# Kernel tuning notes

Measured on AMD Instinct MI355X. Metric: run time of the kernel, lower is better.

The kernel has to match this reference:

```python
import jax, jax.numpy as jnp
import numpy as np

NUM_CLUSTERS = 128  # max cluster id per point cloud (segments per cloud)
EPS = 1e-12         # matches torch F.normalize eps


def setup_inputs() -> dict:
    key = jax.random.key(0)
    k1, k2, k3 = jax.random.split(key, 3)
    K, d, N, M = 64, 320, 2048, NUM_CLUSTERS
    feat = jax.random.normal(k1, (K, d, N), dtype=jnp.float32)
    # binary foreground mask per point (float, as in the torch code: label.float())
    label = (jax.random.uniform(k2, (K, N)) < 0.5).astype(jnp.float32)
    cluster_label = jax.random.randint(k3, (K, N), 0, M, dtype=jnp.int32)
    return {"feat": feat, "label": label, "cluster_label": cluster_label}


def reference(feat, label, cluster_label):
    """Fused aggregate_cluster_one_class + detect_clean_cluster_one_class.

    feat:          (K, d, N) per-point features
    label:         (K, N)    binary class mask (float)
    cluster_label: (K, N)    int cluster ids in [0, NUM_CLUSTERS)
    Returns (cluster_means (K*M, d), sim_score (K*M,), clean_mask (K*M,) float).
    Clusters are laid out as fixed K*M segments; non-class / empty clusters are
    masked out (feature & weight = 0), matching the variable-length gathers of
    the original via masking instead of dynamic shapes.
    """
    K, d, N = feat.shape
    M = NUM_CLUSTERS
    S = K * M

    # Offset cluster ids per cloud -> one flat segment reduce (scatter_add/mean)
    seg = (cluster_label.astype(jnp.int32) + jnp.arange(K, dtype=jnp.int32)[:, None] * M).reshape(-1)  # (K*N,)
    fx = feat.transpose(0, 2, 1).reshape(K * N, d)                     # (K*N, d)

    counts = jax.ops.segment_sum(jnp.ones((K * N,), jnp.float32), seg, num_segments=S)  # scatter_add of ones
    feat_sum = jax.ops.segment_sum(fx, seg, num_segments=S)                              # (S, d)
    lbl_sum = jax.ops.segment_sum(label.reshape(-1), seg, num_segments=S)

    denom = jnp.maximum(counts, 1.0)
    cluster_means = feat_sum / denom[:, None]   # scatter_mean(feat)
    lbl_mean = lbl_sum / denom                  # scatter_mean(label)

    # class clusters: mean label > 0.5 (and cluster non-empty)
    cls_mask = (lbl_mean > 0.5) & (counts > 0)  # (S,) bool

    # ---- detect_clean_cluster_one_class ----
    norm = jnp.linalg.norm(cluster_means, axis=1, keepdims=True)       # L2 over feature dim
    fn = cluster_means / jnp.maximum(norm, EPS)
    fn = jnp.where(cls_mask[:, None], fn, 0.0)                         # drop non-class clusters

    sizes = counts * cls_mask.astype(jnp.float32)
    weight = sizes / jnp.maximum(jnp.max(sizes), 1.0)                  # size / size.max()

    sim_mtx = fn @ fn.T                                                # (S, S) cosine similarities
    sim_score = sim_mtx @ weight                                       # weighted row-sum

    n_valid = jnp.maximum(jnp.sum(cls_mask.astype(jnp.float32)), 1.0)
    mean_score = jnp.sum(sim_score * cls_mask) / n_valid
    clean_mask = (sim_score > mean_score) & cls_mask

    return cluster_means, sim_score, clean_mask.astype(jnp.float32)
```

## Files before the change

kernel.cpp:

```cpp
#include <hip/hip_runtime.h>
#include <hip/hip_bf16.h>

#define KC 64
#define DD 320
#define NP 2048
#define MC 128
#define SS (KC * MC)
#define EPSV 1e-12f

#define CHUNKF 20
#define NCHUNKF 16
#define GFEAT 4
#define NGROUP 5
#define TILEW 2176

__global__ __launch_bounds__(256) void sortstats_kernel(
    const float* __restrict__ label,
    const int* __restrict__ clab,
    unsigned short* __restrict__ spos_ws,
    int* __restrict__ starts_ws,
    float* __restrict__ cls_ws,
    float* __restrict__ sizes_ws,
    unsigned* __restrict__ maxbits,
    float* __restrict__ nvalid)
{
    const int k = blockIdx.x;
    const int tid = threadIdx.x;

    __shared__ int   s_cnt[MC];
    __shared__ float s_lbl[MC];
    __shared__ int   s_scan[MC + 1];
    __shared__ float s_red[256];

    if (tid < MC) { s_cnt[tid] = 0; s_lbl[tid] = 0.f; }
    __syncthreads();

    int id[8], rk[8];
#pragma unroll
    for (int i = 0; i < 8; ++i) {
        const int p = i * 256 + tid;
        id[i] = clab[k * NP + p];
        rk[i] = atomicAdd(&s_cnt[id[i]], 1);
        unsafeAtomicAdd(&s_lbl[id[i]], label[k * NP + p]);
    }
    __syncthreads();

    if (tid < MC) s_scan[tid + 1] = s_cnt[tid];
    if (tid == 0) s_scan[0] = 0;
    __syncthreads();
    for (int off = 1; off < MC; off <<= 1) {
        int v = 0;
        if (tid < MC && (tid + 1) > off) v = s_scan[tid + 1 - off];
        __syncthreads();
        if (tid < MC) s_scan[tid + 1] += v;
        __syncthreads();
    }

    float localmax = 0.f, localval = 0.f;
    if (tid < MC) {
        const int c = s_cnt[tid];
        const float lm = s_lbl[tid] / fmaxf((float)c, 1.f);
        const bool is = (lm > 0.5f) && (c > 0);
        const float sz = is ? (float)c : 0.f;
        cls_ws[k * MC + tid] = is ? 1.f : 0.f;
        sizes_ws[k * MC + tid] = sz;
        localmax = sz;
        localval = is ? 1.f : 0.f;
    }
    s_red[tid] = localmax;
    __syncthreads();
    for (int off = 128; off > 0; off >>= 1) {
        if (tid < off) s_red[tid] = fmaxf(s_red[tid], s_red[tid + off]);
        __syncthreads();
    }
    if (tid == 0) atomicMax(maxbits, __float_as_uint(s_red[0]));
    __syncthreads();
    s_red[tid] = localval;
    __syncthreads();
    for (int off = 128; off > 0; off >>= 1) {
        if (tid < off) s_red[tid] += s_red[tid + off];
        __syncthreads();
    }
    if (tid == 0) unsafeAtomicAdd(nvalid, s_red[0]);

    for (int i = tid; i < MC + 1; i += 256) starts_ws[k * (MC + 1) + i] = s_scan[i];
#pragma unroll
    for (int i = 0; i < 8; ++i) {
        const int p = i * 256 + tid;
        const int sp0 = s_scan[id[i]] + rk[i];
        spos_ws[k * NP + p] = (unsigned short)(sp0 + (sp0 >> 4));
    }
}

__global__ __launch_bounds__(512) void means_kernel(
    const float* __restrict__ feat,
    const unsigned short* __restrict__ spos_ws,
    const int* __restrict__ starts_ws,
    float* __restrict__ means_out)
{
    const int k = blockIdx.x;
    const int chunk = blockIdx.y;
    const int tid = threadIdx.x;

    __shared__ float s_tile[2][GFEAT][TILEW];
    __shared__ unsigned short s_sp[NP];
    __shared__ int s_starts[MC + 1];

    {
        const unsigned* spg = (const unsigned*)(spos_ws + (size_t)k * NP);
        for (int i = tid; i < NP / 2; i += 512) ((unsigned*)s_sp)[i] = spg[i];
        if (tid < MC + 1) s_starts[tid] = starts_ws[k * (MC + 1) + tid];
    }
    __syncthreads();

    const int m = tid & 127;
    const int r = tid >> 7;

    unsigned short sp[16];
#pragma unroll
    for (int q = 0; q < 4; ++q) {
        const int p0 = (m + 128 * q) * 4;
#pragma unroll
        for (int e = 0; e < 4; ++e) sp[4 * q + e] = s_sp[p0 + e];
    }

    const int st = s_starts[m];
    const int en = s_starts[m + 1];
    const float invd = 1.0f / fmaxf((float)(en - st), 1.0f);

    const float* fb = feat + (size_t)k * DD * NP + (size_t)chunk * CHUNKF * NP;
    float regsum[NGROUP];
    float4 ld[4];

    {
        const float4* src = (const float4*)(fb + (size_t)r * NP);
#pragma unroll
        for (int q = 0; q < 4; ++q) ld[q] = src[m + 128 * q];
#pragma unroll
        for (int q = 0; q < 4; ++q) {
            s_tile[0][r][sp[4 * q + 0]] = ld[q].x;
            s_tile[0][r][sp[4 * q + 1]] = ld[q].y;
            s_tile[0][r][sp[4 * q + 2]] = ld[q].z;
            s_tile[0][r][sp[4 * q + 3]] = ld[q].w;
        }
    }
    __syncthreads();

#pragma unroll
    for (int g = 0; g < NGROUP; ++g) {
        const int cur = g & 1;
        if (g + 1 < NGROUP) {
            const float4* src = (const float4*)(fb + (size_t)((g + 1) * GFEAT + r) * NP);
#pragma unroll
            for (int q = 0; q < 4; ++q) ld[q] = src[m + 128 * q];
        }
        float acc = 0.f;
        for (int qq = st; qq < en; ++qq) {
            acc += s_tile[cur][r][qq + (qq >> 4)];
        }
        regsum[g] = acc;
        if (g + 1 < NGROUP) {
#pragma unroll
            for (int q = 0; q < 4; ++q) {
                s_tile[cur ^ 1][r][sp[4 * q + 0]] = ld[q].x;
                s_tile[cur ^ 1][r][sp[4 * q + 1]] = ld[q].y;
                s_tile[cur ^ 1][r][sp[4 * q + 2]] = ld[q].z;
                s_tile[cur ^ 1][r][sp[4 * q + 3]] = ld[q].w;
            }
        }
        __syncthreads();
    }

    float* mrow = means_out + (size_t)(k * MC + m) * DD + chunk * CHUNKF;
#pragma unroll
    for (int g = 0; g < NGROUP; ++g) mrow[g * GFEAT + r] = regsum[g] * invd;
}

__global__ __launch_bounds__(256) void norm_v_kernel(
    const float* __restrict__ means,
    const float* __restrict__ cls,
    const float* __restrict__ sizes,
    const unsigned* __restrict__ maxbits,
    float* __restrict__ rw,
    float* __restrict__ v)
{
    const int wid = threadIdx.x >> 6;
    const int lane = threadIdx.x & 63;
    const int seg0 = blockIdx.x * 64 + wid * 16;
    const float rmx = 1.0f / fmaxf(__uint_as_float(*maxbits), 1.0f);

    float vacc[5] = {0, 0, 0, 0, 0};
    for (int i = 0; i < 16; ++i) {
        const int s = seg0 + i;
        const float* row = means + (size_t)s * DD;
        float val[5];
        float ssum = 0.f;
#pragma unroll
        for (int r = 0; r < 5; ++r) {
            val[r] = row[r * 64 + lane];
            ssum = fmaf(val[r], val[r], ssum);
        }
#pragma unroll
        for (int off = 32; off > 0; off >>= 1) ssum += __shfl_xor(ssum, off, 64);
        const float inv = 1.f / fmaxf(sqrtf(ssum), EPSV);
        const float rwv = cls[s] * inv;
        if (lane == 0) rw[s] = rwv;
        const float coef = sizes[s] * rmx * rwv;
#pragma unroll
        for (int r = 0; r < 5; ++r) vacc[r] = fmaf(coef, val[r], vacc[r]);
    }

    __shared__ float vtmp[4][DD];
#pragma unroll
    for (int r = 0; r < 5; ++r) vtmp[wid][r * 64 + lane] = vacc[r];
    __syncthreads();
    for (int j = threadIdx.x; j < DD; j += 256) {
        unsafeAtomicAdd(&v[j], vtmp[0][j] + vtmp[1][j] + vtmp[2][j] + vtmp[3][j]);
    }
}

__global__ __launch_bounds__(256) void sim_kernel(
    const float* __restrict__ means,
    const float* __restrict__ rw,
    const float* __restrict__ v,
    float* __restrict__ sim_out,
    float* __restrict__ simtotal)
{
    const int wid = threadIdx.x >> 6;
    const int lane = threadIdx.x & 63;
    const int seg0 = blockIdx.x * 64 + wid * 16;

    float vreg[5];
#pragma unroll
    for (int r = 0; r < 5; ++r) vreg[r] = v[r * 64 + lane];

    float lsum = 0.f;
    for (int i = 0; i < 16; ++i) {
        const int s = seg0 + i;
        const float* row = means + (size_t)s * DD;
        float dot = 0.f;
#pragma unroll
        for (int r = 0; r < 5; ++r) dot = fmaf(row[r * 64 + lane], vreg[r], dot);
#pragma unroll
        for (int off = 32; off > 0; off >>= 1) dot += __shfl_xor(dot, off, 64);
        const float sim = rw[s] * dot;
        if (lane == 0) {
            sim_out[s] = sim;
            lsum += sim;
        }
    }
    __shared__ float stmp[4];
    if (lane == 0) stmp[wid] = lsum;
    __syncthreads();
    if (threadIdx.x == 0)
        unsafeAtomicAdd(simtotal, stmp[0] + stmp[1] + stmp[2] + stmp[3]);
}

__global__ __launch_bounds__(256) void clean_kernel(
    const float* __restrict__ sim,
    const float* __restrict__ cls,
    const float* __restrict__ simtotal,
    const float* __restrict__ nvalid,
    float* __restrict__ clean_out)
{
    const float mean = simtotal[0] / fmaxf(nvalid[0], 1.f);
    const int tid = threadIdx.x;
    for (int i = tid; i < SS / 4; i += 256) {
        const float4 s4 = ((const float4*)sim)[i];
        const float4 c4 = ((const float4*)cls)[i];
        float4 o;
        o.x = (s4.x > mean && c4.x != 0.f) ? 1.f : 0.f;
        o.y = (s4.y > mean && c4.y != 0.f) ? 1.f : 0.f;
        o.z = (s4.z > mean && c4.z != 0.f) ? 1.f : 0.f;
        o.w = (s4.w > mean && c4.w != 0.f) ? 1.f : 0.f;
        ((float4*)clean_out)[i] = o;
    }
}

extern "C" void kernel_launch(void* const* d_in, const int* in_sizes, int n_in,
                              void* d_out, int out_size, void* d_ws, size_t ws_size,
                              hipStream_t stream) {
    const float* feat  = (const float*)d_in[0];
    const float* label = (const float*)d_in[1];
    const int*   clab  = (const int*)d_in[2];

    float* out       = (float*)d_out;
    float* means_out = out;
    float* sim_out   = out + (size_t)SS * DD;
    float* clean_out = sim_out + SS;

    float* ws = (float*)d_ws;
    unsigned* maxbits = (unsigned*)&ws[0];
    float* nvalid     = &ws[1];
    float* simtotal   = &ws[2];
    float* v          = &ws[4];
    float* cls        = &ws[352];
    float* sizes      = &ws[352 + SS];
    float* rw         = &ws[352 + 2 * SS];
    int*   starts     = (int*)&ws[352 + 3 * SS];
    unsigned short* spos = (unsigned short*)&ws[352 + 3 * SS + KC * (MC + 1)];

    hipMemsetAsync(d_ws, 0, 324 * sizeof(float), stream);

    sortstats_kernel<<<KC, 256, 0, stream>>>(label, clab, spos, starts,
                                             cls, sizes, maxbits, nvalid);
    means_kernel<<<dim3(KC, NCHUNKF), 512, 0, stream>>>(feat, spos, starts, means_out);
    norm_v_kernel<<<128, 256, 0, stream>>>(means_out, cls, sizes, maxbits, rw, v);
    sim_kernel<<<128, 256, 0, stream>>>(means_out, rw, v, sim_out, simtotal);
    clean_kernel<<<1, 256, 0, stream>>>(sim_out, cls, simtotal, nvalid, clean_out);
}
```

Baseline: 288.9 us.

## Fuse norm, sim and clean kernels into one grid-barrier tail kernel

Replaces the three tail kernels and the workspace memset with a single 128-block kernel. It uses two software grid barriers on atomic counters, and per-block partials replace global atomics for the v vector, the size max, the valid count and the sim total. This removes three launches, a memset and the global atomic contention, and the rw and sim values now stay in registers. In exchange it relies on all 128 blocks being co-resident so the spin barriers cannot deadlock. It also relies on the counters being reset by sortstats before this kernel runs.

```diff
diff --git a/kernel.cpp b/kernel.cpp
--- a/kernel.cpp
+++ b/kernel.cpp
@@ -13,6 +13,8 @@
 #define GFEAT 4
 #define NGROUP 5
 #define TILEW 2176
+
+#define TAILB 128
 
 __global__ __launch_bounds__(256) void sortstats_kernel(
     const float* __restrict__ label,
@@ -21,11 +23,14 @@
     int* __restrict__ starts_ws,
     float* __restrict__ cls_ws,
     float* __restrict__ sizes_ws,
-    unsigned* __restrict__ maxbits,
-    float* __restrict__ nvalid)
+    float* __restrict__ kmax_ws,
+    float* __restrict__ kval_ws,
+    unsigned* __restrict__ counters)
 {
     const int k = blockIdx.x;
     const int tid = threadIdx.x;
+
+    if (k == 0 && tid == 0) { counters[0] = 0u; counters[1] = 0u; }
 
     __shared__ int   s_cnt[MC];
     __shared__ float s_lbl[MC];
@@ -73,7 +78,7 @@
         if (tid < off) s_red[tid] = fmaxf(s_red[tid], s_red[tid + off]);
         __syncthreads();
     }
-    if (tid == 0) atomicMax(maxbits, __float_as_uint(s_red[0]));
+    if (tid == 0) kmax_ws[k] = s_red[0];
     __syncthreads();
     s_red[tid] = localval;
     __syncthreads();
@@ -81,7 +86,7 @@
         if (tid < off) s_red[tid] += s_red[tid + off];
         __syncthreads();
     }
-    if (tid == 0) unsafeAtomicAdd(nvalid, s_red[0]);
+    if (tid == 0) kval_ws[k] = s_red[0];
 
     for (int i = tid; i < MC + 1; i += 256) starts_ws[k * (MC + 1) + i] = s_scan[i];
 #pragma unroll
@@ -176,20 +181,59 @@
     for (int g = 0; g < NGROUP; ++g) mrow[g * GFEAT + r] = regsum[g] * invd;
 }
 
-__global__ __launch_bounds__(256) void norm_v_kernel(
+__device__ inline void grid_barrier(unsigned* cnt, unsigned nblocks) {
+    __syncthreads();
+    if (threadIdx.x == 0) {
+        __hip_atomic_fetch_add(cnt, 1u, __ATOMIC_ACQ_REL, __HIP_MEMORY_SCOPE_AGENT);
+        while (__hip_atomic_load(cnt, __ATOMIC_ACQUIRE, __HIP_MEMORY_SCOPE_AGENT) < nblocks) {
+            __builtin_amdgcn_s_sleep(2);
+        }
+    }
+    __syncthreads();
+}
+
+__global__ __launch_bounds__(256) void tail_kernel(
     const float* __restrict__ means,
     const float* __restrict__ cls,
     const float* __restrict__ sizes,
-    const unsigned* __restrict__ maxbits,
-    float* __restrict__ rw,
-    float* __restrict__ v)
+    const float* __restrict__ kmax,
+    const float* __restrict__ kval,
+    float* __restrict__ vpart,
+    float* __restrict__ simpart,
+    unsigned* __restrict__ counters,
+    float* __restrict__ sim_out,
+    float* __restrict__ clean_out)
 {
-    const int wid = threadIdx.x >> 6;
-    const int lane = threadIdx.x & 63;
-    const int seg0 = blockIdx.x * 64 + wid * 16;
-    const float rmx = 1.0f / fmaxf(__uint_as_float(*maxbits), 1.0f);
-
-    float vacc[5] = {0, 0, 0, 0, 0};
+    const int b = blockIdx.x;
+    const int tid = threadIdx.x;
+    const int wid = tid >> 6;
+    const int lane = tid & 63;
+    const int seg0 = b * 64 + wid * 16;
+
+    __shared__ float vtmp[4][DD];
+    __shared__ float s_v[DD];
+    __shared__ float stmp[4];
+    __shared__ float s_rmx, s_nvalid, s_mean;
+
+    if (wid == 0) {
+        float mv = kmax[lane];
+        float nv = kval[lane];
+#pragma unroll
+        for (int off = 32; off > 0; off >>= 1) {
+            mv = fmaxf(mv, __shfl_xor(mv, off, 64));
+            nv += __shfl_xor(nv, off, 64);
+        }
+        if (lane == 0) {
+            s_rmx = 1.0f / fmaxf(mv, 1.0f);
+            s_nvalid = fmaxf(nv, 1.0f);
+        }
+    }
+    __syncthreads();
+    const float rmx = s_rmx;
+
+    float rw[16];
+    float vacc[5] = {0.f, 0.f, 0.f, 0.f, 0.f};
+#pragma unroll
     for (int i = 0; i < 16; ++i) {
         const int s = seg0 + i;
         const float* row = means + (size_t)s * DD;
@@ -203,38 +247,34 @@
 #pragma unroll
         for (int off = 32; off > 0; off >>= 1) ssum += __shfl_xor(ssum, off, 64);
         const float inv = 1.f / fmaxf(sqrtf(ssum), EPSV);
-        const float rwv = cls[s] * inv;
-        if (lane == 0) rw[s] = rwv;
-        const float coef = sizes[s] * rmx * rwv;
+        rw[i] = cls[s] * inv;
+        const float coef = sizes[s] * rmx * rw[i];
 #pragma unroll
         for (int r = 0; r < 5; ++r) vacc[r] = fmaf(coef, val[r], vacc[r]);
     }
-
-    __shared__ float vtmp[4][DD];
 #pragma unroll
     for (int r = 0; r < 5; ++r) vtmp[wid][r * 64 + lane] = vacc[r];
     __syncthreads();
-    for (int j = threadIdx.x; j < DD; j += 256) {
-        unsafeAtomicAdd(&v[j], vtmp[0][j] + vtmp[1][j] + vtmp[2][j] + vtmp[3][j]);
-    }
-}
-
-__global__ __launch_bounds__(256) void sim_kernel(
-    const float* __restrict__ means,
-    const float* __restrict__ rw,
-    const float* __restrict__ v,
-    float* __restrict__ sim_out,
-    float* __restrict__ simtotal)
-{
-    const int wid = threadIdx.x >> 6;
-    const int lane = threadIdx.x & 63;
-    const int seg0 = blockIdx.x * 64 + wid * 16;
+    for (int j = tid; j < DD; j += 256) {
+        vpart[(size_t)b * DD + j] = vtmp[0][j] + vtmp[1][j] + vtmp[2][j] + vtmp[3][j];
+    }
+
+    grid_barrier(&counters[0], TAILB);
+
+    for (int j = tid; j < DD; j += 256) {
+        float acc = 0.f;
+        for (int bb = 0; bb < TAILB; ++bb) acc += vpart[(size_t)bb * DD + j];
+        s_v[j] = acc;
+    }
+    __syncthreads();
 
     float vreg[5];
 #pragma unroll
-    for (int r = 0; r < 5; ++r) vreg[r] = v[r * 64 + lane];
-
+    for (int r = 0; r < 5; ++r) vreg[r] = s_v[r * 64 + lane];
+
+    float sim[16];
     float lsum = 0.f;
+#pragma unroll
     for (int i = 0; i < 16; ++i) {
         const int s = seg0 + i;
         const float* row = means + (size_t)s * DD;
@@ -243,37 +283,29 @@
         for (int r = 0; r < 5; ++r) dot = fmaf(row[r * 64 + lane], vreg[r], dot);
 #pragma unroll
         for (int off = 32; off > 0; off >>= 1) dot += __shfl_xor(dot, off, 64);
-        const float sim = rw[s] * dot;
-        if (lane == 0) {
-            sim_out[s] = sim;
-            lsum += sim;
-        }
-    }
-    __shared__ float stmp[4];
+        sim[i] = rw[i] * dot;
+        lsum += sim[i];
+        if (lane == 0) sim_out[s] = sim[i];
+    }
     if (lane == 0) stmp[wid] = lsum;
     __syncthreads();
-    if (threadIdx.x == 0)
-        unsafeAtomicAdd(simtotal, stmp[0] + stmp[1] + stmp[2] + stmp[3]);
-}
-
-__global__ __launch_bounds__(256) void clean_kernel(
-    const float* __restrict__ sim,
-    const float* __restrict__ cls,
-    const float* __restrict__ simtotal,
-    const float* __restrict__ nvalid,
-    float* __restrict__ clean_out)
-{
-    const float mean = simtotal[0] / fmaxf(nvalid[0], 1.f);
-    const int tid = threadIdx.x;
-    for (int i = tid; i < SS / 4; i += 256) {
-        const float4 s4 = ((const float4*)sim)[i];
-        const float4 c4 = ((const float4*)cls)[i];
-        float4 o;
-        o.x = (s4.x > mean && c4.x != 0.f) ? 1.f : 0.f;
-        o.y = (s4.y > mean && c4.y != 0.f) ? 1.f : 0.f;
-        o.z = (s4.z > mean && c4.z != 0.f) ? 1.f : 0.f;
-        o.w = (s4.w > mean && c4.w != 0.f) ? 1.f : 0.f;
-        ((float4*)clean_out)[i] = o;
+    if (tid == 0) simpart[b] = stmp[0] + stmp[1] + stmp[2] + stmp[3];
+
+    grid_barrier(&counters[1], TAILB);
+
+    if (wid == 0) {
+        float t = simpart[lane] + simpart[lane + 64];
+#pragma unroll
+        for (int off = 32; off > 0; off >>= 1) t += __shfl_xor(t, off, 64);
+        if (lane == 0) s_mean = t / s_nvalid;
+    }
+    __syncthreads();
+    const float mean = s_mean;
+    if (lane == 0) {
+#pragma unroll
+        for (int i = 0; i < 16; ++i) {
+            clean_out[seg0 + i] = (sim[i] > mean && rw[i] > 0.f) ? 1.f : 0.f;
+        }
     }
 }
 
@@ -290,22 +322,20 @@
     float* clean_out = sim_out + SS;
 
     float* ws = (float*)d_ws;
-    unsigned* maxbits = (unsigned*)&ws[0];
-    float* nvalid     = &ws[1];
-    float* simtotal   = &ws[2];
-    float* v          = &ws[4];
-    float* cls        = &ws[352];
-    float* sizes      = &ws[352 + SS];
-    float* rw         = &ws[352 + 2 * SS];
-    int*   starts     = (int*)&ws[352 + 3 * SS];
-    unsigned short* spos = (unsigned short*)&ws[352 + 3 * SS + KC * (MC + 1)];
-
-    hipMemsetAsync(d_ws, 0, 324 * sizeof(float), stream);
+    unsigned* counters = (unsigned*)&ws[0];
+    float* kmax    = &ws[4];
+    float* kval    = &ws[68];
+    float* simpart = &ws[132];
+    float* vpart   = &ws[260];
+    float* cls     = vpart + TAILB * DD;
+    float* sizes   = cls + SS;
+    int*   starts  = (int*)(sizes + SS);
+    unsigned short* spos = (unsigned short*)(starts + KC * (MC + 1));
 
     sortstats_kernel<<<KC, 256, 0, stream>>>(label, clab, spos, starts,
-                                             cls, sizes, maxbits, nvalid);
+                                             cls, sizes, kmax, kval, counters);
     means_kernel<<<dim3(KC, NCHUNKF), 512, 0, stream>>>(feat, spos, starts, means_out);
-    norm_v_kernel<<<128, 256, 0, stream>>>(means_out, cls, sizes, maxbits, rw, v);
-    sim_kernel<<<128, 256, 0, stream>>>(means_out, rw, v, sim_out, simtotal);
-    clean_kernel<<<1, 256, 0, stream>>>(sim_out, cls, simtotal, nvalid, clean_out);
-}
+    tail_kernel<<<TAILB, 256, 0, stream>>>(means_out, cls, sizes, kmax, kval,
+                                           vpart, simpart, counters,
+                                           sim_out, clean_out);
+}
```

After: 293.2 us. About the same (+1.5%).
